# Kernel optimization log

Measured on AMD Instinct MI355X. Metric: run time of the kernel, lower is better.

Reference implementation:

```python
import jax, jax.numpy as jnp
import numpy as np

B, I, H = 2048, 2048, 2048

def setup_inputs() -> dict:
    key = jax.random.key(0)
    ks = jax.random.split(key, 5)
    # Xavier-ish scale for weights
    W_ih = jax.random.normal(ks[0], (4 * H, I), jnp.float32) * (1.0 / np.sqrt(I))
    W_hh = jax.random.normal(ks[1], (4 * H, H), jnp.float32) * (1.0 / np.sqrt(H))
    b_ih = jnp.zeros((4 * H,), jnp.float32).at[H:2 * H].set(1.0)  # forget bias = 1
    b_hh = jnp.zeros((4 * H,), jnp.float32).at[H:2 * H].set(1.0)
    return {
        "x": jax.random.normal(ks[2], (B, I), jnp.float32),
        "h_prev": jax.random.normal(ks[3], (B, H), jnp.float32),
        "C_prev": jax.random.normal(ks[4], (B, H), jnp.float32),
        "W_ih": W_ih, "b_ih": b_ih, "W_hh": W_hh, "b_hh": b_hh,
    }

def reference(x, h_prev, C_prev, W_ih, b_ih, W_hh, b_hh):
    # Two GEMMs producing pre-activations for all four gates: [B, 4H]
    gates = jnp.dot(x, W_ih.T) + b_ih + jnp.dot(h_prev, W_hh.T) + b_hh
    gi, gf, gg, go = jnp.split(gates, 4, axis=1)  # torch chunk order: i, f, g, o
    input_gate = jax.nn.sigmoid(gi)
    forget_gate = jax.nn.sigmoid(gf)
    candidate_gate = jnp.tanh(gg)
    output_gate = jax.nn.sigmoid(go)
    new_C = forget_gate * C_prev + input_gate * candidate_gate
    new_h = output_gate * jnp.tanh(new_C)
    return (new_h, new_C, forget_gate, input_gate, candidate_gate, output_gate)
```

## Files before the change

kernel.cpp:

```cpp
#include <hip/hip_runtime.h>
#include <cstdint>
#include <cstddef>


typedef __attribute__((ext_vector_type(8))) short bf16x8;
typedef __attribute__((ext_vector_type(4))) float f32x4;

#define GLD_AS1 const __attribute__((address_space(1))) void
#define GLD_AS3 __attribute__((address_space(3))) void

__device__ __forceinline__ void gload_lds16(const void* g, void* l) {
  __builtin_amdgcn_global_load_lds((GLD_AS1*)g, (GLD_AS3*)l, 16, 0, 0);
}

__device__ __forceinline__ unsigned short f2bf(float f) {
  unsigned int u = __float_as_uint(f);
  unsigned int r = 0x7FFFu + ((u >> 16) & 1u);
  return (unsigned short)((u + r) >> 16);
}

__device__ __forceinline__ void barrier_f() {
  asm volatile("" ::: "memory");
  __builtin_amdgcn_s_barrier();
  asm volatile("" ::: "memory");
}

__device__ __forceinline__ float sigm(float x) { return 1.0f / (1.0f + __expf(-x)); }

__global__ __launch_bounds__(256) void cvt_all(const float* __restrict__ x,
                                               const float* __restrict__ h,
                                               const float* __restrict__ Wih,
                                               const float* __restrict__ Whh,
                                               unsigned short* __restrict__ Abf,
                                               unsigned short* __restrict__ Wbf) {
  int bid = blockIdx.x;
  const float* src; unsigned short* dst; int col_off; int base;
  if (bid < 4096)        { src = x;   dst = Abf; col_off = 0;    base = bid; }
  else if (bid < 8192)   { src = h;   dst = Abf; col_off = 2048; base = bid - 4096; }
  else if (bid < 24576)  { src = Wih; dst = Wbf; col_off = 0;    base = bid - 8192; }
  else                   { src = Whh; dst = Wbf; col_off = 2048; base = bid - 24576; }
  int i = base * 256 + threadIdx.x;
  int flat = i << 2;
  int r = flat >> 11;
  int c = flat & 2047;
  float4 v = *(const float4*)(src + flat);
  ushort4 o;
  o.x = f2bf(v.x); o.y = f2bf(v.y); o.z = f2bf(v.z); o.w = f2bf(v.w);
  *(ushort4*)(dst + (((size_t)r) << 12) + col_off + c) = o;
}

__global__ __launch_bounds__(512, 2) void gemm_lstm(
    const unsigned short* __restrict__ A,
    const unsigned short* __restrict__ W,
    const float* __restrict__ b_ih, const float* __restrict__ b_hh,
    const float* __restrict__ C_prev,
    float* __restrict__ out)
{
  constexpr int K = 4096;
  constexpr int BK = 64;
  constexpr int NT = K / BK;
  __shared__ alignas(16) unsigned short lds[2][4][128 * 64];

  int b  = blockIdx.x;
  int xc = b & 7, ii = b >> 3;
  int bm = (ii & 7) * 256;
  int h0 = (xc * 4 + (ii >> 3)) * 64;

  int tid  = threadIdx.x;
  int lane = tid & 63;
  int w    = tid >> 6;
  int wm   = w >> 2;
  int wn   = w & 3;
  int l15  = lane & 15;
  int lq   = lane >> 4;

  int ce0 = ((lq * 16) ^ ((l15 & 7) << 4)) >> 1;
  int ce1 = ((64 + lq * 16) ^ ((l15 & 7) << 4)) >> 1;

  int srow_s = lane >> 3;
  int scol = ((lane & 7) ^ (lane >> 3)) * 8;
  const unsigned short* gA = A + (size_t)(bm + 16 * w + srow_s) * K + scol;
  const unsigned short* gB0 =
      W + (size_t)((w & 3) * 2048 + h0 + 16 * (w >> 2) + srow_s) * K + scol;

  f32x4 acc[8][4] = {};

  auto stageA = [&](int t, int hh) {
    unsigned short* l0 = &lds[t & 1][hh][w * 1024];
    const unsigned short* g = gA + (size_t)hh * 128 * K + t * BK;
    gload_lds16(g, l0);
    gload_lds16(g + (size_t)8 * K, l0 + 512);
  };
  auto stageB = [&](int t, int hh) {
    unsigned short* l0 = &lds[t & 1][2 + hh][w * 1024];
    const unsigned short* g = gB0 + (size_t)hh * 32 * K + t * BK;
    gload_lds16(g, l0);
    gload_lds16(g + (size_t)8 * K, l0 + 512);
  };

  stageA(0, 0); stageA(0, 1); stageB(0, 0); stageB(0, 1);
  stageA(1, 0); stageA(1, 1); stageB(1, 0); stageB(1, 1);

  bf16x8 af[4][2], bf01[2][2], bf23[2][2];

  for (int t = 0; t < NT; ++t) {
    if (t < NT - 1) asm volatile("s_waitcnt vmcnt(8)" ::: "memory");
    else            asm volatile("s_waitcnt vmcnt(0)" ::: "memory");
    barrier_f();

    const unsigned short* Ab = lds[t & 1][wm];
    const unsigned short* Bb = lds[t & 1][2 + (wn >> 1)];
    int brow = (wn & 1) * 64;

#pragma unroll
    for (int mt = 0; mt < 4; ++mt) {
      af[mt][0] = *(const bf16x8*)&Ab[(mt * 16 + l15) * 64 + ce0];
      af[mt][1] = *(const bf16x8*)&Ab[(mt * 16 + l15) * 64 + ce1];
    }
#pragma unroll
    for (int nt = 0; nt < 2; ++nt) {
      bf01[nt][0] = *(const bf16x8*)&Bb[(brow + nt * 16 + l15) * 64 + ce0];
      bf01[nt][1] = *(const bf16x8*)&Bb[(brow + nt * 16 + l15) * 64 + ce1];
    }
    barrier_f();
    __builtin_amdgcn_s_setprio(1);
#pragma unroll
    for (int mt = 0; mt < 4; ++mt)
#pragma unroll
      for (int nt = 0; nt < 2; ++nt) {
        acc[mt][nt] = __builtin_amdgcn_mfma_f32_16x16x32_bf16(af[mt][0], bf01[nt][0], acc[mt][nt], 0, 0, 0);
        acc[mt][nt] = __builtin_amdgcn_mfma_f32_16x16x32_bf16(af[mt][1], bf01[nt][1], acc[mt][nt], 0, 0, 0);
      }
    __builtin_amdgcn_s_setprio(0);
    barrier_f();

#pragma unroll
    for (int nt = 0; nt < 2; ++nt) {
      bf23[nt][0] = *(const bf16x8*)&Bb[(brow + (2 + nt) * 16 + l15) * 64 + ce0];
      bf23[nt][1] = *(const bf16x8*)&Bb[(brow + (2 + nt) * 16 + l15) * 64 + ce1];
    }
    barrier_f();
    __builtin_amdgcn_s_setprio(1);
#pragma unroll
    for (int mt = 0; mt < 4; ++mt)
#pragma unroll
      for (int nt = 0; nt < 2; ++nt) {
        acc[mt][2 + nt] = __builtin_amdgcn_mfma_f32_16x16x32_bf16(af[mt][0], bf23[nt][0], acc[mt][2 + nt], 0, 0, 0);
        acc[mt][2 + nt] = __builtin_amdgcn_mfma_f32_16x16x32_bf16(af[mt][1], bf23[nt][1], acc[mt][2 + nt], 0, 0, 0);
      }
    __builtin_amdgcn_s_setprio(0);
    barrier_f();

#pragma unroll
    for (int mt = 0; mt < 4; ++mt) {
      af[mt][0] = *(const bf16x8*)&Ab[(64 + mt * 16 + l15) * 64 + ce0];
      af[mt][1] = *(const bf16x8*)&Ab[(64 + mt * 16 + l15) * 64 + ce1];
    }
    if (t + 2 < NT) { stageB(t + 2, 0); stageB(t + 2, 1); }
    barrier_f();
    __builtin_amdgcn_s_setprio(1);
#pragma unroll
    for (int mt = 0; mt < 4; ++mt)
#pragma unroll
      for (int nt = 0; nt < 2; ++nt) {
        acc[4 + mt][2 + nt] = __builtin_amdgcn_mfma_f32_16x16x32_bf16(af[mt][0], bf23[nt][0], acc[4 + mt][2 + nt], 0, 0, 0);
        acc[4 + mt][2 + nt] = __builtin_amdgcn_mfma_f32_16x16x32_bf16(af[mt][1], bf23[nt][1], acc[4 + mt][2 + nt], 0, 0, 0);
      }
    __builtin_amdgcn_s_setprio(0);
    barrier_f();

    if (t + 2 < NT) { stageA(t + 2, 0); stageA(t + 2, 1); }
    barrier_f();
    __builtin_amdgcn_s_setprio(1);
#pragma unroll
    for (int mt = 0; mt < 4; ++mt)
#pragma unroll
      for (int nt = 0; nt < 2; ++nt) {
        acc[4 + mt][nt] = __builtin_amdgcn_mfma_f32_16x16x32_bf16(af[mt][0], bf01[nt][0], acc[4 + mt][nt], 0, 0, 0);
        acc[4 + mt][nt] = __builtin_amdgcn_mfma_f32_16x16x32_bf16(af[mt][1], bf01[nt][1], acc[4 + mt][nt], 0, 0, 0);
      }
    __builtin_amdgcn_s_setprio(0);
  }

  int hcol = h0 + wn * 16 + l15;
  float cb0 = b_ih[hcol]          + b_hh[hcol];
  float cb1 = b_ih[2048 + hcol]   + b_hh[2048 + hcol];
  float cb2 = b_ih[4096 + hcol]   + b_hh[4096 + hcol];
  float cb3 = b_ih[6144 + hcol]   + b_hh[6144 + hcol];
  constexpr size_t SEC = (size_t)2048 * 2048;
#pragma unroll
  for (int mt = 0; mt < 8; ++mt) {
    int row0 = bm + wm * 128 + mt * 16 + lq * 4;
#pragma unroll
    for (int j = 0; j < 4; ++j) {
      size_t off = (size_t)(row0 + j) * 2048 + hcol;
      float I = sigm(acc[mt][0][j] + cb0);
      float F = sigm(acc[mt][1][j] + cb1);
      float G = tanhf(acc[mt][2][j] + cb2);
      float O = sigm(acc[mt][3][j] + cb3);
      float C = F * C_prev[off] + I * G;
      float H = O * tanhf(C);
      out[0 * SEC + off] = H;
      out[1 * SEC + off] = C;
      out[2 * SEC + off] = F;
      out[3 * SEC + off] = I;
      out[4 * SEC + off] = G;
      out[5 * SEC + off] = O;
    }
  }
}

extern "C" void kernel_launch(void* const* d_in, const int* in_sizes, int n_in,
                              void* d_out, int out_size, void* d_ws, size_t ws_size,
                              hipStream_t stream) {
  const float* x   = (const float*)d_in[0];
  const float* h   = (const float*)d_in[1];
  const float* Cp  = (const float*)d_in[2];
  const float* Wih = (const float*)d_in[3];
  const float* bih = (const float*)d_in[4];
  const float* Whh = (const float*)d_in[5];
  const float* bhh = (const float*)d_in[6];
  float* out = (float*)d_out;

  uint8_t* ws = (uint8_t*)d_ws;
  unsigned short* Abf  = (unsigned short*)ws;
  unsigned short* Wbf  = (unsigned short*)(ws + (size_t)(16u << 20));

  cvt_all<<<40960, 256, 0, stream>>>(x, h, Wih, Whh, Abf, Wbf);
  gemm_lstm<<<256, 512, 0, stream>>>(Abf, Wbf, bih, bhh, Cp, out);
}
```

Measured before the change: 190.6 us.

## Fuse fp32-to-bf16 weight conversion into GEMM B-tile loading

The separate conversion pass over the 128 MB of fp32 weights is removed. The GEMM now loads fp32 weight tiles into registers, packs them to bf16 with v_cvt_pk_bf16_f32, and writes them to LDS, prefetching two stages ahead. The inner loop is also reorganised with fewer barriers and merged B-fragment reads. Each weight tile is now re-read in fp32 by every M-block (8 of them), which doubles global weight traffic per block and adds register pressure and VALU conversion work inside the main loop.

```diff
diff --git a/kernel.cpp b/kernel.cpp
--- a/kernel.cpp
+++ b/kernel.cpp
@@ -25,20 +25,24 @@
   asm volatile("" ::: "memory");
 }
 
+__device__ __forceinline__ uint4 pk8(float4 a, float4 b) {
+  uint4 d;
+  asm("v_cvt_pk_bf16_f32 %0, %1, %2" : "=v"(d.x) : "v"(a.x), "v"(a.y));
+  asm("v_cvt_pk_bf16_f32 %0, %1, %2" : "=v"(d.y) : "v"(a.z), "v"(a.w));
+  asm("v_cvt_pk_bf16_f32 %0, %1, %2" : "=v"(d.z) : "v"(b.x), "v"(b.y));
+  asm("v_cvt_pk_bf16_f32 %0, %1, %2" : "=v"(d.w) : "v"(b.z), "v"(b.w));
+  return d;
+}
+
 __device__ __forceinline__ float sigm(float x) { return 1.0f / (1.0f + __expf(-x)); }
 
-__global__ __launch_bounds__(256) void cvt_all(const float* __restrict__ x,
-                                               const float* __restrict__ h,
-                                               const float* __restrict__ Wih,
-                                               const float* __restrict__ Whh,
-                                               unsigned short* __restrict__ Abf,
-                                               unsigned short* __restrict__ Wbf) {
+__global__ __launch_bounds__(256) void cvt_A(const float* __restrict__ x,
+                                             const float* __restrict__ h,
+                                             unsigned short* __restrict__ Abf) {
   int bid = blockIdx.x;
-  const float* src; unsigned short* dst; int col_off; int base;
-  if (bid < 4096)        { src = x;   dst = Abf; col_off = 0;    base = bid; }
-  else if (bid < 8192)   { src = h;   dst = Abf; col_off = 2048; base = bid - 4096; }
-  else if (bid < 24576)  { src = Wih; dst = Wbf; col_off = 0;    base = bid - 8192; }
-  else                   { src = Whh; dst = Wbf; col_off = 2048; base = bid - 24576; }
+  const float* src; int col_off; int base;
+  if (bid < 4096) { src = x; col_off = 0;    base = bid; }
+  else            { src = h; col_off = 2048; base = bid - 4096; }
   int i = base * 256 + threadIdx.x;
   int flat = i << 2;
   int r = flat >> 11;
@@ -46,12 +50,13 @@
   float4 v = *(const float4*)(src + flat);
   ushort4 o;
   o.x = f2bf(v.x); o.y = f2bf(v.y); o.z = f2bf(v.z); o.w = f2bf(v.w);
-  *(ushort4*)(dst + (((size_t)r) << 12) + col_off + c) = o;
+  *(ushort4*)(Abf + (((size_t)r) << 12) + col_off + c) = o;
 }
 
 __global__ __launch_bounds__(512, 2) void gemm_lstm(
     const unsigned short* __restrict__ A,
-    const unsigned short* __restrict__ W,
+    const float* __restrict__ Wih,
+    const float* __restrict__ Whh,
     const float* __restrict__ b_ih, const float* __restrict__ b_hh,
     const float* __restrict__ C_prev,
     float* __restrict__ out)
@@ -73,17 +78,18 @@
   int wn   = w & 3;
   int l15  = lane & 15;
   int lq   = lane >> 4;
+  int sr3  = lane >> 3;
+  int l7   = lane & 7;
 
   int ce0 = ((lq * 16) ^ ((l15 & 7) << 4)) >> 1;
   int ce1 = ((64 + lq * 16) ^ ((l15 & 7) << 4)) >> 1;
 
-  int srow_s = lane >> 3;
-  int scol = ((lane & 7) ^ (lane >> 3)) * 8;
-  const unsigned short* gA = A + (size_t)(bm + 16 * w + srow_s) * K + scol;
-  const unsigned short* gB0 =
-      W + (size_t)((w & 3) * 2048 + h0 + 16 * (w >> 2) + srow_s) * K + scol;
+  int scol = (l7 ^ sr3) * 8;
+  const unsigned short* gA = A + (size_t)(bm + 16 * w + sr3) * K + scol;
+  int bWrow = (w & 3) * 2048 + h0 + 16 * (w >> 2) + sr3;
 
   f32x4 acc[8][4] = {};
+  float4 bl[8];
 
   auto stageA = [&](int t, int hh) {
     unsigned short* l0 = &lds[t & 1][hh][w * 1024];
@@ -91,23 +97,45 @@
     gload_lds16(g, l0);
     gload_lds16(g + (size_t)8 * K, l0 + 512);
   };
-  auto stageB = [&](int t, int hh) {
-    unsigned short* l0 = &lds[t & 1][2 + hh][w * 1024];
-    const unsigned short* g = gB0 + (size_t)hh * 32 * K + t * BK;
-    gload_lds16(g, l0);
-    gload_lds16(g + (size_t)8 * K, l0 + 512);
+  auto loadB = [&](int tt) {
+    const float* Wsel = (tt < 32) ? Wih : Whh;
+    const float* gw = Wsel + (size_t)bWrow * 2048 + (tt & 31) * BK + scol;
+#pragma unroll
+    for (int p = 0; p < 2; ++p)
+#pragma unroll
+      for (int i = 0; i < 2; ++i) {
+        const float* g = gw + (size_t)(32 * p + 8 * i) * 2048;
+        bl[p * 4 + i * 2 + 0] = *(const float4*)(g);
+        bl[p * 4 + i * 2 + 1] = *(const float4*)(g + 4);
+      }
   };
-
-  stageA(0, 0); stageA(0, 1); stageB(0, 0); stageB(0, 1);
-  stageA(1, 0); stageA(1, 1); stageB(1, 0); stageB(1, 1);
+  auto writeB = [&](int t) {
+#pragma unroll
+    for (int p = 0; p < 2; ++p)
+#pragma unroll
+      for (int i = 0; i < 2; ++i) {
+        uint4 d = pk8(bl[p * 4 + i * 2 + 0], bl[p * 4 + i * 2 + 1]);
+        *(uint4*)&lds[t & 1][2 + p][(16 * w + 8 * i + sr3) * 64 + l7 * 8] = d;
+      }
+  };
+
+  loadB(0);
+  asm volatile("" ::: "memory");
+  stageA(0, 0); stageA(0, 1);
+  asm volatile("" ::: "memory");
+  asm volatile("s_waitcnt vmcnt(4)" ::: "memory");
+  writeB(0);
+  loadB(1);
+  asm volatile("" ::: "memory");
+  stageA(1, 0); stageA(1, 1);
+  asm volatile("" ::: "memory");
+  asm volatile("s_waitcnt vmcnt(12)" ::: "memory");
+  asm volatile("s_waitcnt lgkmcnt(0)" ::: "memory");
+  barrier_f();
 
   bf16x8 af[4][2], bf01[2][2], bf23[2][2];
 
   for (int t = 0; t < NT; ++t) {
-    if (t < NT - 1) asm volatile("s_waitcnt vmcnt(8)" ::: "memory");
-    else            asm volatile("s_waitcnt vmcnt(0)" ::: "memory");
-    barrier_f();
-
     const unsigned short* Ab = lds[t & 1][wm];
     const unsigned short* Bb = lds[t & 1][2 + (wn >> 1)];
     int brow = (wn & 1) * 64;
@@ -121,8 +149,10 @@
     for (int nt = 0; nt < 2; ++nt) {
       bf01[nt][0] = *(const bf16x8*)&Bb[(brow + nt * 16 + l15) * 64 + ce0];
       bf01[nt][1] = *(const bf16x8*)&Bb[(brow + nt * 16 + l15) * 64 + ce1];
-    }
-    barrier_f();
+      bf23[nt][0] = *(const bf16x8*)&Bb[(brow + (2 + nt) * 16 + l15) * 64 + ce0];
+      bf23[nt][1] = *(const bf16x8*)&Bb[(brow + (2 + nt) * 16 + l15) * 64 + ce1];
+    }
+
     __builtin_amdgcn_s_setprio(1);
 #pragma unroll
     for (int mt = 0; mt < 4; ++mt)
@@ -130,34 +160,26 @@
       for (int nt = 0; nt < 2; ++nt) {
         acc[mt][nt] = __builtin_amdgcn_mfma_f32_16x16x32_bf16(af[mt][0], bf01[nt][0], acc[mt][nt], 0, 0, 0);
         acc[mt][nt] = __builtin_amdgcn_mfma_f32_16x16x32_bf16(af[mt][1], bf01[nt][1], acc[mt][nt], 0, 0, 0);
-      }
-    __builtin_amdgcn_s_setprio(0);
-    barrier_f();
-
-#pragma unroll
-    for (int nt = 0; nt < 2; ++nt) {
-      bf23[nt][0] = *(const bf16x8*)&Bb[(brow + (2 + nt) * 16 + l15) * 64 + ce0];
-      bf23[nt][1] = *(const bf16x8*)&Bb[(brow + (2 + nt) * 16 + l15) * 64 + ce1];
-    }
-    barrier_f();
-    __builtin_amdgcn_s_setprio(1);
-#pragma unroll
-    for (int mt = 0; mt < 4; ++mt)
-#pragma unroll
-      for (int nt = 0; nt < 2; ++nt) {
         acc[mt][2 + nt] = __builtin_amdgcn_mfma_f32_16x16x32_bf16(af[mt][0], bf23[nt][0], acc[mt][2 + nt], 0, 0, 0);
         acc[mt][2 + nt] = __builtin_amdgcn_mfma_f32_16x16x32_bf16(af[mt][1], bf23[nt][1], acc[mt][2 + nt], 0, 0, 0);
       }
     __builtin_amdgcn_s_setprio(0);
-    barrier_f();
 
 #pragma unroll
     for (int mt = 0; mt < 4; ++mt) {
       af[mt][0] = *(const bf16x8*)&Ab[(64 + mt * 16 + l15) * 64 + ce0];
       af[mt][1] = *(const bf16x8*)&Ab[(64 + mt * 16 + l15) * 64 + ce1];
     }
-    if (t + 2 < NT) { stageB(t + 2, 0); stageB(t + 2, 1); }
+
     barrier_f();
+
+    if (t < NT - 1) {
+      asm volatile("s_waitcnt vmcnt(4)" ::: "memory");
+      writeB(t + 1);
+    }
+    if (t + 2 < NT) loadB(t + 2);
+    asm volatile("" ::: "memory");
+
     __builtin_amdgcn_s_setprio(1);
 #pragma unroll
     for (int mt = 0; mt < 4; ++mt)
@@ -167,10 +189,10 @@
         acc[4 + mt][2 + nt] = __builtin_amdgcn_mfma_f32_16x16x32_bf16(af[mt][1], bf23[nt][1], acc[4 + mt][2 + nt], 0, 0, 0);
       }
     __builtin_amdgcn_s_setprio(0);
+
     barrier_f();
-
     if (t + 2 < NT) { stageA(t + 2, 0); stageA(t + 2, 1); }
-    barrier_f();
+
     __builtin_amdgcn_s_setprio(1);
 #pragma unroll
     for (int mt = 0; mt < 4; ++mt)
@@ -180,13 +202,20 @@
         acc[4 + mt][nt] = __builtin_amdgcn_mfma_f32_16x16x32_bf16(af[mt][1], bf01[nt][1], acc[4 + mt][nt], 0, 0, 0);
       }
     __builtin_amdgcn_s_setprio(0);
+
+    if (t < NT - 1) {
+      asm volatile("s_waitcnt lgkmcnt(0)" ::: "memory");
+      if (t < NT - 2) asm volatile("s_waitcnt vmcnt(12)" ::: "memory");
+      else            asm volatile("s_waitcnt vmcnt(0)" ::: "memory");
+      barrier_f();
+    }
   }
 
   int hcol = h0 + wn * 16 + l15;
-  float cb0 = b_ih[hcol]          + b_hh[hcol];
-  float cb1 = b_ih[2048 + hcol]   + b_hh[2048 + hcol];
-  float cb2 = b_ih[4096 + hcol]   + b_hh[4096 + hcol];
-  float cb3 = b_ih[6144 + hcol]   + b_hh[6144 + hcol];
+  float cb0 = b_ih[hcol]        + b_hh[hcol];
+  float cb1 = b_ih[2048 + hcol] + b_hh[2048 + hcol];
+  float cb2 = b_ih[4096 + hcol] + b_hh[4096 + hcol];
+  float cb3 = b_ih[6144 + hcol] + b_hh[6144 + hcol];
   constexpr size_t SEC = (size_t)2048 * 2048;
 #pragma unroll
   for (int mt = 0; mt < 8; ++mt) {
@@ -222,10 +251,8 @@
   const float* bhh = (const float*)d_in[6];
   float* out = (float*)d_out;
 
-  uint8_t* ws = (uint8_t*)d_ws;
-  unsigned short* Abf  = (unsigned short*)ws;
-  unsigned short* Wbf  = (unsigned short*)(ws + (size_t)(16u << 20));
-
-  cvt_all<<<40960, 256, 0, stream>>>(x, h, Wih, Whh, Abf, Wbf);
-  gemm_lstm<<<256, 512, 0, stream>>>(Abf, Wbf, bih, bhh, Cp, out);
-}
+  unsigned short* Abf = (unsigned short*)d_ws;
+
+  cvt_A<<<8192, 256, 0, stream>>>(x, h, Abf);
+  gemm_lstm<<<256, 512, 0, stream>>>(Abf, Wih, Whh, bih, bhh, Cp, out);
+}
```

New measurement: 195.6 us. 2.6% more time.
